# Performance work log

Measured on AMD Instinct MI355X. Metric: run time of the kernel, lower is better.

## Reference

```python
import jax, jax.numpy as jnp
import numpy as np

IN_CH = 1024
HID_CH = 1024
NUM_HEADS = 16
HEAD_DIM = HID_CH // NUM_HEADS
SCALE = (HID_CH / NUM_HEADS) ** (-0.25)


def _xavier(key, shape):
    fan_out, fan_in = shape
    limit = np.sqrt(6.0 / (fan_in + fan_out)).astype(np.float32)
    return jax.random.uniform(key, shape, jnp.float32, -limit, limit)


def setup_inputs() -> dict:
    key = jax.random.key(0)
    ks = jax.random.split(key, 5)
    B, T, L = 4, 2048, 512
    inpt = jax.random.normal(ks[0], (B, IN_CH, T), jnp.float32)
    aux = jax.random.normal(ks[1], (L, IN_CH), jnp.float32)
    q_w = _xavier(ks[2], (HID_CH, IN_CH))
    q_b = jnp.zeros((HID_CH,), jnp.float32)
    kv_w = _xavier(ks[3], (2 * HID_CH, IN_CH))
    kv_b = jnp.zeros((2 * HID_CH,), jnp.float32)
    out_w = _xavier(ks[4], (IN_CH, HID_CH))
    out_b = jnp.zeros((IN_CH,), jnp.float32)
    return {"inpt": inpt, "aux": aux, "q_w": q_w, "q_b": q_b,
            "kv_w": kv_w, "kv_b": kv_b, "out_w": out_w, "out_b": out_b}


def reference(inpt, aux, q_w, q_b, kv_w, kv_b, out_w, out_b):
    # inpt: (B, C, T), aux: (L, C)
    B, C, T = inpt.shape
    x = jnp.swapaxes(inpt, -2, -1)                     # (B, T, C)
    q = (x @ q_w.T + q_b) * SCALE                      # (B, T, H*D)
    kv = aux @ kv_w.T + kv_b                           # (L, 2*H*D)
    k, v = jnp.split(kv, 2, axis=-1)
    k = k * SCALE
    q = q.reshape(B, T, NUM_HEADS, HEAD_DIM)           # (B, T, h, d)
    L = aux.shape[0]
    k = k.reshape(L, NUM_HEADS, HEAD_DIM)              # (L, h, d)
    v = v.reshape(L, NUM_HEADS, HEAD_DIM)
    e = jnp.einsum('bihd,jhd->bijh', q, k)             # (B, T, L, h)
    attn = jax.nn.softmax(e, axis=2)                   # softmax over key axis j
    out = jnp.einsum('bijh,jhd->bihd', attn, v)        # (B, T, h, d)
    out = out.reshape(B, T, HID_CH) @ out_w.T + out_b  # (B, T, C)
    return inpt + jnp.swapaxes(out, -2, -1)            # (B, C, T)
```

## Files before the change

### kernel.cpp

```cpp
#include <hip/hip_runtime.h>
#include <cstdint>
#include <cstddef>

typedef __bf16 bf16;
typedef __bf16 bf16x4 __attribute__((ext_vector_type(4)));
typedef __bf16 bf16x8 __attribute__((ext_vector_type(8)));
typedef float f32x4 __attribute__((ext_vector_type(4)));

static constexpr float SCALE_F = 0.35355339059327373f;

#define AS1 __attribute__((address_space(1)))
#define AS3 __attribute__((address_space(3)))

__device__ __forceinline__ void load_lds16(const void* g, void* l) {
  __builtin_amdgcn_global_load_lds((AS1 void*)g, (AS3 void*)l, 16, 0, 0);
}


__global__ void cvt_all(const float* __restrict__ a, bf16* __restrict__ oa,
                        const float* __restrict__ b, bf16* __restrict__ ob,
                        const float* __restrict__ c, bf16* __restrict__ oc,
                        const float* __restrict__ d, bf16* __restrict__ od) {
  int i = blockIdx.x * blockDim.x + threadIdx.x;
  const float* src;
  bf16* dst;
  int off;
  if (i < 262144) { src = a; dst = oa; off = i; }
  else if (i < 786432) { src = b; dst = ob; off = i - 262144; }
  else if (i < 1048576) { src = c; dst = oc; off = i - 786432; }
  else { src = d; dst = od; off = i - 1048576; }
  float4 v = reinterpret_cast<const float4*>(src)[off];
  bf16x4 o;
  o[0] = (bf16)v.x; o[1] = (bf16)v.y; o[2] = (bf16)v.z; o[3] = (bf16)v.w;
  reinterpret_cast<bf16x4*>(dst)[off] = o;
}

__global__ void transpose_in(const float* __restrict__ inpt, bf16* __restrict__ X) {
  __shared__ float tile[32][33];
  int b = blockIdx.z;
  int t0 = blockIdx.x * 32, c0 = blockIdx.y * 32;
  int tx = threadIdx.x, ty = threadIdx.y;
  const float* src = inpt + ((size_t)b * 1024 + c0) * 2048 + t0;
#pragma unroll
  for (int i = 0; i < 4; ++i) tile[ty + i * 8][tx] = src[(size_t)(ty + i * 8) * 2048 + tx];
  __syncthreads();
  bf16* dst = X + ((size_t)b * 2048 + t0) * 1024 + c0;
#pragma unroll
  for (int i = 0; i < 4; ++i) dst[(size_t)(ty + i * 8) * 1024 + tx] = (bf16)tile[tx][ty + i * 8];
}

__global__ void residual_out(const float* __restrict__ inpt, const bf16* __restrict__ Z,
                             float* __restrict__ out) {
  __shared__ float tile[32][33];
  int b = blockIdx.z;
  int t0 = blockIdx.x * 32, c0 = blockIdx.y * 32;
  int tx = threadIdx.x, ty = threadIdx.y;
  const bf16* zsrc = Z + ((size_t)b * 2048 + t0) * 1024 + c0;
#pragma unroll
  for (int i = 0; i < 4; ++i) tile[ty + i * 8][tx] = (float)zsrc[(size_t)(ty + i * 8) * 1024 + tx];
  __syncthreads();
  size_t ob = ((size_t)b * 1024 + c0) * 2048 + t0;
#pragma unroll
  for (int i = 0; i < 4; ++i) {
    size_t idx = ob + (size_t)(ty + i * 8) * 2048 + tx;
    out[idx] = inpt[idx] + tile[tx][ty + i * 8];
  }
}


__global__ __launch_bounds__(256, 2) void gemm_qkv(
    const bf16* __restrict__ X, const bf16* __restrict__ qwb, const float* __restrict__ q_b,
    bf16* __restrict__ Qout, const bf16* __restrict__ auxb, const bf16* __restrict__ kvwb,
    const float* __restrict__ kv_b, bf16* __restrict__ Kout, bf16* __restrict__ Vout) {
  __shared__ __align__(16) char sA[16384];
  __shared__ __align__(16) char sB[16384];
  const int tid = threadIdx.x;
  const int lane = tid & 63;
  const int wave = tid >> 6;
  const int wm = wave >> 1, wn = wave & 1;
  const int bid = blockIdx.x;
  const bool isQ = bid < 512;
  const bf16 *A, *Bw;
  const float* bias;
  int m0, n0;
  if (isQ) {
    A = X; Bw = qwb; bias = q_b;
    m0 = (bid >> 3) * 128; n0 = (bid & 7) * 128;
  } else {
    int b2 = bid - 512;
    A = auxb; Bw = kvwb; bias = kv_b;
    m0 = (b2 & 3) * 128; n0 = (b2 >> 2) * 128;
  }
  f32x4 acc[4][4] = {};

  for (int kt = 0; kt < 1024; kt += 64) {
#pragma unroll
    for (int j = 0; j < 4; ++j) {
      int i = tid + j * 256;
      int r = i >> 3, q = i & 7;
      int so = (q ^ (r & 7)) << 4;
      load_lds16((const char*)(A + (size_t)(m0 + r) * 1024 + kt) + so, sA + (size_t)i * 16);
      load_lds16((const char*)(Bw + (size_t)(n0 + r) * 1024 + kt) + so, sB + (size_t)i * 16);
    }
    asm volatile("s_waitcnt vmcnt(0)" ::: "memory");
    __syncthreads();
    bf16x8 af[4][2], bfr[4][2];
#pragma unroll
    for (int mi = 0; mi < 4; ++mi)
#pragma unroll
      for (int kk = 0; kk < 2; ++kk) {
        int rr = wm * 64 + mi * 16 + (lane & 15);
        int w = kk * 64 + ((lane >> 4) << 4);
        af[mi][kk] = *(const bf16x8*)(sA + (size_t)rr * 128 + (w ^ ((rr & 7) << 4)));
        int r2 = wn * 64 + mi * 16 + (lane & 15);
        bfr[mi][kk] = *(const bf16x8*)(sB + (size_t)r2 * 128 + (w ^ ((r2 & 7) << 4)));
      }
#pragma unroll
    for (int kk = 0; kk < 2; ++kk)
#pragma unroll
      for (int mi = 0; mi < 4; ++mi)
#pragma unroll
        for (int ni = 0; ni < 4; ++ni)
          acc[mi][ni] =
              __builtin_amdgcn_mfma_f32_16x16x32_bf16(af[mi][kk], bfr[ni][kk], acc[mi][ni], 0, 0, 0);
    __syncthreads();
  }

  float bs[4];
#pragma unroll
  for (int ni = 0; ni < 4; ++ni) bs[ni] = bias[n0 + wn * 64 + ni * 16 + (lane & 15)];

#pragma unroll
  for (int mi = 0; mi < 4; ++mi)
#pragma unroll
    for (int ni = 0; ni < 4; ++ni)
#pragma unroll
      for (int j = 0; j < 4; ++j) {
        int row = wm * 64 + mi * 16 + ((lane >> 4) << 2) + j;
        int col = wn * 64 + ni * 16 + (lane & 15);
        int m = m0 + row, n = n0 + col;
        float val = acc[mi][ni][j] + bs[ni];
        if (isQ) {
          val *= SCALE_F;
          int bb = m >> 11, t = m & 2047, hh = n >> 6, d = n & 63;
          Qout[(((size_t)(bb * 16 + hh) * 2048 + t) << 6) + d] = (bf16)val;
        } else {
          if (n < 1024) {
            int hh = n >> 6, d = n & 63;
            Kout[(((size_t)hh * 512 + m) << 6) + d] = (bf16)(val * SCALE_F);
          } else {
            int n2 = n - 1024;
            int hh = n2 >> 6, d = n2 & 63;
            Vout[(((size_t)hh * 64 + d) << 9) + m] = (bf16)val;
          }
        }
      }
}

__global__ __launch_bounds__(256, 2) void gemm_out(const bf16* __restrict__ A,
                                                   const bf16* __restrict__ Bw,
                                                   const float* __restrict__ bias,
                                                   bf16* __restrict__ out0) {
  __shared__ __align__(16) char sA[16384];
  __shared__ __align__(16) char sB[16384];
  const int tid = threadIdx.x;
  const int lane = tid & 63;
  const int wave = tid >> 6;
  const int wm = wave >> 1, wn = wave & 1;
  const int m0 = blockIdx.x * 128, n0 = blockIdx.y * 128;
  f32x4 acc[4][4] = {};

  for (int kt = 0; kt < 1024; kt += 64) {
#pragma unroll
    for (int j = 0; j < 4; ++j) {
      int i = tid + j * 256;
      int r = i >> 3, q = i & 7;
      int so = (q ^ (r & 7)) << 4;
      load_lds16((const char*)(A + (size_t)(m0 + r) * 1024 + kt) + so, sA + (size_t)i * 16);
      load_lds16((const char*)(Bw + (size_t)(n0 + r) * 1024 + kt) + so, sB + (size_t)i * 16);
    }
    asm volatile("s_waitcnt vmcnt(0)" ::: "memory");
    __syncthreads();
    bf16x8 af[4][2], bfr[4][2];
#pragma unroll
    for (int mi = 0; mi < 4; ++mi)
#pragma unroll
      for (int kk = 0; kk < 2; ++kk) {
        int rr = wm * 64 + mi * 16 + (lane & 15);
        int w = kk * 64 + ((lane >> 4) << 4);
        af[mi][kk] = *(const bf16x8*)(sA + (size_t)rr * 128 + (w ^ ((rr & 7) << 4)));
        int r2 = wn * 64 + mi * 16 + (lane & 15);
        bfr[mi][kk] = *(const bf16x8*)(sB + (size_t)r2 * 128 + (w ^ ((r2 & 7) << 4)));
      }
#pragma unroll
    for (int kk = 0; kk < 2; ++kk)
#pragma unroll
      for (int mi = 0; mi < 4; ++mi)
#pragma unroll
        for (int ni = 0; ni < 4; ++ni)
          acc[mi][ni] =
              __builtin_amdgcn_mfma_f32_16x16x32_bf16(af[mi][kk], bfr[ni][kk], acc[mi][ni], 0, 0, 0);
    __syncthreads();
  }

  float bs[4];
#pragma unroll
  for (int ni = 0; ni < 4; ++ni) bs[ni] = bias[n0 + wn * 64 + ni * 16 + (lane & 15)];
#pragma unroll
  for (int mi = 0; mi < 4; ++mi)
#pragma unroll
    for (int ni = 0; ni < 4; ++ni)
#pragma unroll
      for (int j = 0; j < 4; ++j) {
        int row = wm * 64 + mi * 16 + ((lane >> 4) << 2) + j;
        int col = wn * 64 + ni * 16 + (lane & 15);
        out0[(size_t)(m0 + row) * 1024 + n0 + col] = (bf16)(acc[mi][ni][j] + bs[ni]);
      }
}

__global__ __launch_bounds__(512, 4) void attn_kernel(const bf16* __restrict__ Q,
                                                      const bf16* __restrict__ Kw,
                                                      const bf16* __restrict__ Vt,
                                                      bf16* __restrict__ Y) {
  __shared__ __align__(16) char lds[75776];
  const int tid = threadIdx.x;
  const int lane = tid & 63;
  const int wv = tid >> 6;
  const int g = lane >> 4;
  const int lr = lane & 15;
  const int t0 = blockIdx.x * 64;
  const int bh = blockIdx.y;
  const int b = bh >> 4, h = bh & 15;

  const bf16* Kh = Kw + (size_t)h * 512 * 64;
  bf16x8 ka[2][4];
#pragma unroll
  for (int kk = 0; kk < 2; ++kk)
#pragma unroll
    for (int mi = 0; mi < 4; ++mi) {
      int key = wv * 64 + mi * 16 + lr;
      ka[kk][mi] = *(const bf16x8*)((const char*)Kh + (size_t)key * 128 + kk * 64 + g * 16);
    }

  {
    const bf16* Qh = Q + ((size_t)(b * 16 + h) * 2048 + t0) * 64;
    int r = tid >> 3, c = tid & 7;
    load_lds16((const char*)Qh + r * 128 + ((c * 16) ^ ((r & 7) << 4)),
               lds + 65536 + (size_t)tid * 16);
  }
  asm volatile("s_waitcnt vmcnt(0)" ::: "memory");
  __syncthreads();

  float psum[4];
#pragma unroll
  for (int ni = 0; ni < 4; ++ni) {
    int q = ni * 16 + lr;
    f32x4 acc[4] = {};
#pragma unroll
    for (int kk = 0; kk < 2; ++kk) {
      bf16x8 qb = *(const bf16x8*)(lds + 65536 + (size_t)q * 128 +
                                   ((kk * 64 + g * 16) ^ ((q & 7) << 4)));
#pragma unroll
      for (int mi = 0; mi < 4; ++mi)
        acc[mi] = __builtin_amdgcn_mfma_f32_16x16x32_bf16(ka[kk][mi], qb, acc[mi], 0, 0, 0);
    }
    float ps = 0.f;
#pragma unroll
    for (int mi = 0; mi < 4; ++mi) {
      bf16x4 w;
#pragma unroll
      for (int j = 0; j < 4; ++j) {
        float p = __expf(acc[mi][j] - 16.0f);
        ps += p;
        w[j] = (bf16)p;
      }
      *(bf16x4*)(lds + (size_t)q * 1024 + ((wv * 128 + mi * 32 + g * 8) ^ ((q & 7) << 4))) = w;
    }
    ps += __shfl_xor(ps, 16);
    ps += __shfl_xor(ps, 32);
    psum[ni] = ps;
  }
  if (lane < 16) {
#pragma unroll
    for (int ni = 0; ni < 4; ++ni)
      *(float*)(lds + 73728 + (((ni * 16 + lr) * 8 + wv) << 2)) = psum[ni];
  }

  const bf16* Vh = Vt + (size_t)h * 64 * 512;
  const int mi_o = wv >> 1;
  const int d = mi_o * 16 + lr;
  bf16x8 va[16];
#pragma unroll
  for (int kk = 0; kk < 16; ++kk)
    va[kk] = *(const bf16x8*)((const char*)Vh + (size_t)d * 1024 + kk * 64 + g * 16);
  __syncthreads();

  const int q0 = (wv & 1) * 32 + lr, q1 = q0 + 16;
  f32x4 o0 = {}, o1 = {};
#pragma unroll
  for (int kk = 0; kk < 16; ++kk) {
    bf16x8 p0 = *(const bf16x8*)(lds + (size_t)q0 * 1024 + ((kk * 64 + g * 16) ^ ((q0 & 7) << 4)));
    bf16x8 p1 = *(const bf16x8*)(lds + (size_t)q1 * 1024 + ((kk * 64 + g * 16) ^ ((q1 & 7) << 4)));
    o0 = __builtin_amdgcn_mfma_f32_16x16x32_bf16(va[kk], p0, o0, 0, 0, 0);
    o1 = __builtin_amdgcn_mfma_f32_16x16x32_bf16(va[kk], p1, o1, 0, 0, 0);
  }
  __syncthreads();

  f32x4 sa0 = *(const f32x4*)(lds + 73728 + q0 * 32);
  f32x4 sb0 = *(const f32x4*)(lds + 73728 + q0 * 32 + 16);
  f32x4 sa1 = *(const f32x4*)(lds + 73728 + q1 * 32);
  f32x4 sb1 = *(const f32x4*)(lds + 73728 + q1 * 32 + 16);
  float s0v = ((sa0[0] + sa0[1]) + (sa0[2] + sa0[3])) + ((sb0[0] + sb0[1]) + (sb0[2] + sb0[3]));
  float s1v = ((sa1[0] + sa1[1]) + (sa1[2] + sa1[3])) + ((sb1[0] + sb1[1]) + (sb1[2] + sb1[3]));

  {
    float i0 = 1.0f / s0v, i1 = 1.0f / s1v;
    int byt = mi_o * 64 + g * 16;
    f32x4 w0, w1;
#pragma unroll
    for (int j = 0; j < 4; ++j) {
      w0[j] = o0[j] * i0;
      w1[j] = o1[j] * i1;
    }
    *(f32x4*)(lds + (size_t)q0 * 256 + (byt ^ ((q0 & 7) << 4))) = w0;
    *(f32x4*)(lds + (size_t)q1 * 256 + (byt ^ ((q1 & 7) << 4))) = w1;
  }
  __syncthreads();

  {
    int q = tid >> 3, sub = tid & 7;
    int base = sub * 32;
    f32x4 a = *(const f32x4*)(lds + (size_t)q * 256 + (base ^ ((q & 7) << 4)));
    f32x4 c = *(const f32x4*)(lds + (size_t)q * 256 + ((base + 16) ^ ((q & 7) << 4)));
    bf16x8 w;
#pragma unroll
    for (int j = 0; j < 4; ++j) {
      w[j] = (bf16)a[j];
      w[4 + j] = (bf16)c[j];
    }
    *(bf16x8*)((char*)Y + (((size_t)(b * 2048 + t0 + q) * 1024 + h * 64 + sub * 8) * 2)) = w;
  }
}


extern "C" void kernel_launch(void* const* d_in, const int* in_sizes, int n_in, void* d_out,
                              int out_size, void* d_ws, size_t ws_size, hipStream_t stream) {
  const float* inpt = (const float*)d_in[0];
  const float* aux = (const float*)d_in[1];
  const float* q_w = (const float*)d_in[2];
  const float* q_b = (const float*)d_in[3];
  const float* kv_w = (const float*)d_in[4];
  const float* kv_b = (const float*)d_in[5];
  const float* out_w = (const float*)d_in[6];
  const float* out_b = (const float*)d_in[7];
  float* out = (float*)d_out;
  char* ws = (char*)d_ws;
  bf16* X = (bf16*)(ws + 0);
  bf16* QZ = (bf16*)(ws + (16u << 20));
  bf16* qwb = (bf16*)(ws + (32u << 20));
  bf16* kvwb = (bf16*)(ws + (34u << 20));
  bf16* owb = (bf16*)(ws + (38u << 20));
  bf16* auxb = (bf16*)(ws + (40u << 20));
  bf16* Kws = (bf16*)(ws + (41u << 20));
  bf16* Vtw = (bf16*)(ws + (42u << 20));

  cvt_all<<<4608, 256, 0, stream>>>(q_w, qwb, kv_w, kvwb, out_w, owb, aux, auxb);
  transpose_in<<<dim3(64, 32, 4), dim3(32, 8), 0, stream>>>(inpt, X);

  gemm_qkv<<<576, 256, 0, stream>>>(X, qwb, q_b, QZ, auxb, kvwb, kv_b, Kws, Vtw);
  attn_kernel<<<dim3(32, 64), 512, 0, stream>>>(QZ, Kws, Vtw, X );
  gemm_out<<<dim3(64, 8), 256, 0, stream>>>(X, owb, out_b, QZ );
  residual_out<<<dim3(64, 32, 4), dim3(32, 8), 0, stream>>>(inpt, QZ, out);
}
```

Baseline: 222.7 us.

## Restructure attention to stage full K/V per head in LDS and stream key groups

The attention kernel now loads one head's entire K and V (each 64 KB) into LDS once per block. Each block handles 512 queries, and every wave keeps 64 queries in registers. Each wave walks the 512 keys in groups of 32, computing scores, exp and the PV product in registers with double-buffered fragment loads. This replaces the old per-64-query blocks that wrote probabilities to LDS and re-read V from global memory. V's key axis is permuted in the QKV GEMM epilogue so the P fragments from score MFMAs can be fed directly as PV operands. This removes the LDS round-trips and repeated K/V loads, at the cost of 128 KB LDS per block and a smaller grid of 256 blocks with lower occupancy.

```diff
diff --git a/kernel.cpp b/kernel.cpp
--- a/kernel.cpp
+++ b/kernel.cpp
@@ -151,7 +151,8 @@
           } else {
             int n2 = n - 1024;
             int hh = n2 >> 6, d = n2 & 63;
-            Vout[(((size_t)hh * 64 + d) << 9) + m] = (bf16)val;
+            int sl = (m & 0x1E0) | (((m >> 2) & 3) << 3) | (((m >> 4) & 1) << 2) | (m & 3);
+            Vout[(((size_t)hh * 64 + d) << 9) + sl] = (bf16)val;
           }
         }
       }
@@ -218,127 +219,121 @@
       }
 }
 
-__global__ __launch_bounds__(512, 4) void attn_kernel(const bf16* __restrict__ Q,
+struct Frags {
+  bf16x8 ka[2][2];
+  bf16x8 va[4];
+};
+
+__device__ __forceinline__ void load_frags(Frags& f, const char* lds, int G, int lr, int g) {
+  const int swz = (lr & 7) << 4;
+#pragma unroll
+  for (int m = 0; m < 2; ++m)
+#pragma unroll
+    for (int kk = 0; kk < 2; ++kk)
+      f.ka[m][kk] =
+          *(const bf16x8*)(lds + (size_t)(G * 32 + m * 16 + lr) * 128 + ((kk * 64 + g * 16) ^ swz));
+#pragma unroll
+  for (int db = 0; db < 4; ++db)
+    f.va[db] = *(const bf16x8*)(lds + 65536 + (size_t)(db * 16 + lr) * 1024 +
+                                ((G * 64 + g * 16) ^ swz));
+}
+
+__device__ __forceinline__ void compute_group(const Frags& f, const bf16x8 (&qf)[4][2],
+                                              f32x4 (&oacc)[4][4], float (&psum)[4]) {
+  f32x4 sa[4][2] = {};
+#pragma unroll
+  for (int s = 0; s < 4; ++s)
+#pragma unroll
+    for (int m = 0; m < 2; ++m) {
+      sa[s][m] = __builtin_amdgcn_mfma_f32_16x16x32_bf16(f.ka[m][0], qf[s][0], sa[s][m], 0, 0, 0);
+      sa[s][m] = __builtin_amdgcn_mfma_f32_16x16x32_bf16(f.ka[m][1], qf[s][1], sa[s][m], 0, 0, 0);
+    }
+  bf16x8 pb[4];
+#pragma unroll
+  for (int s = 0; s < 4; ++s)
+#pragma unroll
+    for (int m = 0; m < 2; ++m)
+#pragma unroll
+      for (int j = 0; j < 4; ++j) {
+        float p = __expf(sa[s][m][j] - 16.0f);
+        psum[s] += p;
+        pb[s][m * 4 + j] = (bf16)p;
+      }
+#pragma unroll
+  for (int s = 0; s < 4; ++s)
+#pragma unroll
+    for (int db = 0; db < 4; ++db)
+      oacc[s][db] = __builtin_amdgcn_mfma_f32_16x16x32_bf16(f.va[db], pb[s], oacc[s][db], 0, 0, 0);
+}
+
+__global__ __launch_bounds__(512, 2) void attn_kernel(const bf16* __restrict__ Q,
                                                       const bf16* __restrict__ Kw,
                                                       const bf16* __restrict__ Vt,
                                                       bf16* __restrict__ Y) {
-  __shared__ __align__(16) char lds[75776];
+  __shared__ __align__(16) char lds[131072];
   const int tid = threadIdx.x;
   const int lane = tid & 63;
   const int wv = tid >> 6;
-  const int g = lane >> 4;
-  const int lr = lane & 15;
-  const int t0 = blockIdx.x * 64;
-  const int bh = blockIdx.y;
-  const int b = bh >> 4, h = bh & 15;
+  const int g = lane >> 4, lr = lane & 15;
+  const int bix = blockIdx.x;
+  const int b = bix >> 6, h = (bix >> 2) & 15, tc = bix & 3;
 
   const bf16* Kh = Kw + (size_t)h * 512 * 64;
-  bf16x8 ka[2][4];
-#pragma unroll
-  for (int kk = 0; kk < 2; ++kk)
-#pragma unroll
-    for (int mi = 0; mi < 4; ++mi) {
-      int key = wv * 64 + mi * 16 + lr;
-      ka[kk][mi] = *(const bf16x8*)((const char*)Kh + (size_t)key * 128 + kk * 64 + g * 16);
-    }
-
-  {
-    const bf16* Qh = Q + ((size_t)(b * 16 + h) * 2048 + t0) * 64;
-    int r = tid >> 3, c = tid & 7;
-    load_lds16((const char*)Qh + r * 128 + ((c * 16) ^ ((r & 7) << 4)),
-               lds + 65536 + (size_t)tid * 16);
-  }
+  const bf16* Vh = Vt + (size_t)h * 64 * 512;
+#pragma unroll
+  for (int j = 0; j < 8; ++j) {
+    int i = tid + j * 512;
+    int r = i >> 3, c = i & 7;
+    load_lds16((const char*)Kh + r * 128 + ((c * 16) ^ ((r & 7) << 4)), lds + (size_t)i * 16);
+  }
+#pragma unroll
+  for (int j = 0; j < 8; ++j) {
+    int i = tid + j * 512;
+    int r = i >> 6, c = i & 63;
+    load_lds16((const char*)Vh + r * 1024 + ((c * 16) ^ ((r & 7) << 4)),
+               lds + 65536 + (size_t)i * 16);
+  }
+
+  const int tb = tc * 512 + wv * 64;
+  const bf16* Qh = Q + ((size_t)(b * 16 + h) * 2048 + tb) * 64;
+  bf16x8 qf[4][2];
+#pragma unroll
+  for (int s = 0; s < 4; ++s)
+#pragma unroll
+    for (int kk = 0; kk < 2; ++kk)
+      qf[s][kk] = *(const bf16x8*)((const char*)Qh + (s * 16 + lr) * 128 + kk * 64 + g * 16);
+
   asm volatile("s_waitcnt vmcnt(0)" ::: "memory");
   __syncthreads();
 
-  float psum[4];
-#pragma unroll
-  for (int ni = 0; ni < 4; ++ni) {
-    int q = ni * 16 + lr;
-    f32x4 acc[4] = {};
-#pragma unroll
-    for (int kk = 0; kk < 2; ++kk) {
-      bf16x8 qb = *(const bf16x8*)(lds + 65536 + (size_t)q * 128 +
-                                   ((kk * 64 + g * 16) ^ ((q & 7) << 4)));
-#pragma unroll
-      for (int mi = 0; mi < 4; ++mi)
-        acc[mi] = __builtin_amdgcn_mfma_f32_16x16x32_bf16(ka[kk][mi], qb, acc[mi], 0, 0, 0);
+  f32x4 oacc[4][4] = {};
+  float psum[4] = {};
+
+  Frags fA, fB;
+  load_frags(fA, lds, 0, lr, g);
+#pragma unroll 1
+  for (int G = 0; G < 16; G += 2) {
+    load_frags(fB, lds, G + 1, lr, g);
+    compute_group(fA, qf, oacc, psum);
+    if (G + 2 < 16) load_frags(fA, lds, G + 2, lr, g);
+    compute_group(fB, qf, oacc, psum);
+  }
+
+#pragma unroll
+  for (int s = 0; s < 4; ++s) {
+    float ssum = psum[s];
+    ssum += __shfl_xor(ssum, 16);
+    ssum += __shfl_xor(ssum, 32);
+    float inv = 1.0f / ssum;
+    int t = tb + s * 16 + lr;
+    char* yrow = (char*)Y + ((size_t)(b * 2048 + t) * 1024 + h * 64) * 2;
+#pragma unroll
+    for (int db = 0; db < 4; ++db) {
+      bf16x4 w;
+#pragma unroll
+      for (int j = 0; j < 4; ++j) w[j] = (bf16)(oacc[s][db][j] * inv);
+      *(bf16x4*)(yrow + (db * 16 + g * 4) * 2) = w;
     }
-    float ps = 0.f;
-#pragma unroll
-    for (int mi = 0; mi < 4; ++mi) {
-      bf16x4 w;
-#pragma unroll
-      for (int j = 0; j < 4; ++j) {
-        float p = __expf(acc[mi][j] - 16.0f);
-        ps += p;
-        w[j] = (bf16)p;
-      }
-      *(bf16x4*)(lds + (size_t)q * 1024 + ((wv * 128 + mi * 32 + g * 8) ^ ((q & 7) << 4))) = w;
-    }
-    ps += __shfl_xor(ps, 16);
-    ps += __shfl_xor(ps, 32);
-    psum[ni] = ps;
-  }
-  if (lane < 16) {
-#pragma unroll
-    for (int ni = 0; ni < 4; ++ni)
-      *(float*)(lds + 73728 + (((ni * 16 + lr) * 8 + wv) << 2)) = psum[ni];
-  }
-
-  const bf16* Vh = Vt + (size_t)h * 64 * 512;
-  const int mi_o = wv >> 1;
-  const int d = mi_o * 16 + lr;
-  bf16x8 va[16];
-#pragma unroll
-  for (int kk = 0; kk < 16; ++kk)
-    va[kk] = *(const bf16x8*)((const char*)Vh + (size_t)d * 1024 + kk * 64 + g * 16);
-  __syncthreads();
-
-  const int q0 = (wv & 1) * 32 + lr, q1 = q0 + 16;
-  f32x4 o0 = {}, o1 = {};
-#pragma unroll
-  for (int kk = 0; kk < 16; ++kk) {
-    bf16x8 p0 = *(const bf16x8*)(lds + (size_t)q0 * 1024 + ((kk * 64 + g * 16) ^ ((q0 & 7) << 4)));
-    bf16x8 p1 = *(const bf16x8*)(lds + (size_t)q1 * 1024 + ((kk * 64 + g * 16) ^ ((q1 & 7) << 4)));
-    o0 = __builtin_amdgcn_mfma_f32_16x16x32_bf16(va[kk], p0, o0, 0, 0, 0);
-    o1 = __builtin_amdgcn_mfma_f32_16x16x32_bf16(va[kk], p1, o1, 0, 0, 0);
-  }
-  __syncthreads();
-
-  f32x4 sa0 = *(const f32x4*)(lds + 73728 + q0 * 32);
-  f32x4 sb0 = *(const f32x4*)(lds + 73728 + q0 * 32 + 16);
-  f32x4 sa1 = *(const f32x4*)(lds + 73728 + q1 * 32);
-  f32x4 sb1 = *(const f32x4*)(lds + 73728 + q1 * 32 + 16);
-  float s0v = ((sa0[0] + sa0[1]) + (sa0[2] + sa0[3])) + ((sb0[0] + sb0[1]) + (sb0[2] + sb0[3]));
-  float s1v = ((sa1[0] + sa1[1]) + (sa1[2] + sa1[3])) + ((sb1[0] + sb1[1]) + (sb1[2] + sb1[3]));
-
-  {
-    float i0 = 1.0f / s0v, i1 = 1.0f / s1v;
-    int byt = mi_o * 64 + g * 16;
-    f32x4 w0, w1;
-#pragma unroll
-    for (int j = 0; j < 4; ++j) {
-      w0[j] = o0[j] * i0;
-      w1[j] = o1[j] * i1;
-    }
-    *(f32x4*)(lds + (size_t)q0 * 256 + (byt ^ ((q0 & 7) << 4))) = w0;
-    *(f32x4*)(lds + (size_t)q1 * 256 + (byt ^ ((q1 & 7) << 4))) = w1;
-  }
-  __syncthreads();
-
-  {
-    int q = tid >> 3, sub = tid & 7;
-    int base = sub * 32;
-    f32x4 a = *(const f32x4*)(lds + (size_t)q * 256 + (base ^ ((q & 7) << 4)));
-    f32x4 c = *(const f32x4*)(lds + (size_t)q * 256 + ((base + 16) ^ ((q & 7) << 4)));
-    bf16x8 w;
-#pragma unroll
-    for (int j = 0; j < 4; ++j) {
-      w[j] = (bf16)a[j];
-      w[4 + j] = (bf16)c[j];
-    }
-    *(bf16x8*)((char*)Y + (((size_t)(b * 2048 + t0 + q) * 1024 + h * 64 + sub * 8) * 2)) = w;
   }
 }
 
@@ -368,7 +363,7 @@
   transpose_in<<<dim3(64, 32, 4), dim3(32, 8), 0, stream>>>(inpt, X);
 
   gemm_qkv<<<576, 256, 0, stream>>>(X, qwb, q_b, QZ, auxb, kvwb, kv_b, Kws, Vtw);
-  attn_kernel<<<dim3(32, 64), 512, 0, stream>>>(QZ, Kws, Vtw, X );
+  attn_kernel<<<256, 512, 0, stream>>>(QZ, Kws, Vtw, X );
   gemm_out<<<dim3(64, 8), 256, 0, stream>>>(X, owb, out_b, QZ );
   residual_out<<<dim3(64, 32, 4), dim3(32, 8), 0, stream>>>(inpt, QZ, out);
 }
```

Result: faster. 205.6 us (-7.7%).
